# Kernel optimization log

Hardware: AMD Instinct MI355X
Metric: run time of the kernel (lower is better)

## Reference

```python
import jax, jax.numpy as jnp
import numpy as np

_EPS = 1e-6
_ZCA_EPS = 1e-5
NEG_SLOPE_ATTN = 0.2   # LeakyReLU inside score_mlp
NEG_SLOPE_FFN = 0.1    # VNLinearLeakyReLU negative_slope


def _safe_norm(x, axis, keepdims=False):
    # norm with zero-gradient at exactly-zero vectors (matches torch subgradient)
    sq = jnp.sum(x * x, axis=axis, keepdims=keepdims)
    safe = jnp.where(sq == 0, 1.0, sq)
    return jnp.sqrt(safe) * (sq > 0)


def vn_linear(W, x):
    # W: (out, in); x: (B, C_in, 3, N) -> (B, C_out, 3, N)
    return jnp.einsum('oi,bivn->bovn', W, x)


def zca_layernorm(x, gamma):
    # x: (B, C, 3, N); whiten the 3D vector components per batch element
    B, C = x.shape[0], x.shape[1]
    xf = x.reshape(B, C, 3, -1).transpose(0, 2, 1, 3).reshape(B, 3, -1)
    xf = xf.astype(jnp.float32)
    mu = xf.mean(axis=-1, keepdims=True)
    xc = xf - mu
    M = xc.shape[-1]
    cov = (xc @ xc.transpose(0, 2, 1)) / (float(M) + _EPS)  # (B,3,3)
    cov = cov + _ZCA_EPS * jnp.eye(3, dtype=cov.dtype)[None]
    w, V = jnp.linalg.eigh(cov)
    w = jnp.maximum(w, _ZCA_EPS)
    Wm = (V * jax.lax.rsqrt(w)[:, None, :]) @ V.transpose(0, 2, 1)  # (B,3,3)
    xw = Wm @ xc
    xw = xw.reshape(B, 3, C, -1).transpose(0, 2, 1, 3).reshape(x.shape).astype(x.dtype)
    return xw * gamma[None, :, None, None]


def cwsa_attention(x, pos, Wq, Wk, Wv, Wo, W1, b1, W2, b2):
    q = vn_linear(Wq, x)  # (B,C,3,N)
    k = vn_linear(Wk, x)
    v = vn_linear(Wv, x)
    qk = q.transpose(0, 3, 1, 2)  # (B,N,C,3)
    kk = k.transpose(0, 3, 1, 2)
    vv = v.transpose(0, 3, 1, 2)
    rel = qk[:, :, None, :, :] - kk[:, None, :, :, :]      # (B,N,N,C,3)
    rel_norm = _safe_norm(rel, axis=-1)                    # (B,N,N,C)
    rel_mean = rel_norm.mean(axis=-1, keepdims=True)       # (B,N,N,1)
    rel_pos = pos[:, :, None, :] - pos[:, None, :, :]      # (B,N,N,3)
    rel_pos_norm = _safe_norm(rel_pos, axis=-1, keepdims=True)  # (B,N,N,1)
    score_in = jnp.concatenate([rel_mean, rel_pos_norm], axis=-1)  # (B,N,N,2)
    h = jax.nn.leaky_relu(score_in @ W1.T + b1, NEG_SLOPE_ATTN)
    scores = h @ W2.T + b2                                  # (B,N,N,C)
    attn = jax.nn.softmax(scores, axis=2)                   # softmax over keys j
    out = jnp.einsum('bijk,bjkd->bikd', attn, vv)           # (B,N,C,3)
    out = out.transpose(0, 2, 3, 1)                         # (B,C,3,N)
    return vn_linear(Wo, out)


def vn_leaky_relu(p, d, ns):
    # p, d: (B, C, 3, N)
    dot = jnp.sum(p * d, axis=2, keepdims=True)
    dsq = jnp.sum(d * d, axis=2, keepdims=True)
    mask = (dot >= 0).astype(p.dtype)
    proj = p - (dot / (dsq + _EPS)) * d
    return ns * p + (1.0 - ns) * (mask * p + (1.0 - mask) * proj)


def ffn(x, Wfeat, Wdir, Wffn2):
    p = vn_linear(Wfeat, x)
    d = vn_linear(Wdir, x)
    h = vn_leaky_relu(p, d, NEG_SLOPE_FFN)
    return vn_linear(Wffn2, h)


def setup_inputs() -> dict:
    key = jax.random.key(0)
    ks = jax.random.split(key, 16)
    B, C, N = 2, 128, 256
    hidden, ratio = 64, 2
    sC = 1.0 / np.sqrt(C)
    inp = {
        'x': jax.random.normal(ks[0], (B, C, 3, N), dtype=jnp.float32),
        'pos': jax.random.normal(ks[1], (B, N, 3), dtype=jnp.float32),
        'Wq': jax.random.normal(ks[2], (C, C), dtype=jnp.float32) * sC,
        'Wk': jax.random.normal(ks[3], (C, C), dtype=jnp.float32) * sC,
        'Wv': jax.random.normal(ks[4], (C, C), dtype=jnp.float32) * sC,
        'Wo': jax.random.normal(ks[5], (C, C), dtype=jnp.float32) * sC,
        'W1': jax.random.normal(ks[6], (hidden, 2), dtype=jnp.float32) * (1.0 / np.sqrt(2.0)),
        'b1': jnp.zeros((hidden,), dtype=jnp.float32),
        'W2': jax.random.normal(ks[7], (C, hidden), dtype=jnp.float32) * (1.0 / np.sqrt(hidden)),
        'b2': jnp.zeros((C,), dtype=jnp.float32),
        'gamma1': jnp.ones((C,), dtype=jnp.float32),
        'Wfeat': jax.random.normal(ks[8], (C * ratio, C), dtype=jnp.float32) * sC,
        'Wdir': jax.random.normal(ks[9], (C * ratio, C), dtype=jnp.float32) * sC,
        'Wffn2': jax.random.normal(ks[10], (C, C * ratio), dtype=jnp.float32) * (1.0 / np.sqrt(C * ratio)),
        'gamma2': jnp.ones((C,), dtype=jnp.float32),
    }
    return inp


def reference(x, pos, Wq, Wk, Wv, Wo, W1, b1, W2, b2, gamma1, Wfeat, Wdir, Wffn2, gamma2):
    a = cwsa_attention(x, pos, Wq, Wk, Wv, Wo, W1, b1, W2, b2)
    x1 = zca_layernorm(x + a, gamma1)
    f = ffn(x1, Wfeat, Wdir, Wffn2)
    return zca_layernorm(x1 + f, gamma2)
```

## Files before the change

kernel.cpp:

```cpp
#include <hip/hip_runtime.h>
#include <math.h>

#define BB 2
#define CC 128
#define NN 256
#define HH 64
#define CHX 256
#define COLS 768
#define NEG_ATTN 0.2f
#define NEG_FFN 0.1f

typedef __attribute__((ext_vector_type(8))) short short8b;
typedef __attribute__((ext_vector_type(4))) float f32x4;

__device__ __forceinline__ unsigned bf16rne(float x) {
  unsigned u = __float_as_uint(x);
  return (u + 0x7fffu + ((u >> 16) & 1u)) >> 16;
}

__global__ __launch_bounds__(256) void k_qkv(
    const float* __restrict__ x, const float* __restrict__ Wq,
    const float* __restrict__ Wk, const float* __restrict__ Wv,
    float* __restrict__ q_t, float* __restrict__ k_nat, float* __restrict__ v_t3)
{
  const int ct = blockIdx.x, which = blockIdx.y, b = blockIdx.z;
  const int col0 = ct * 16;
  __shared__ float xt[CC][16];
  const float* xb = x + (size_t)b * CC * COLS;
  for (int idx = threadIdx.x; idx < CC * 16; idx += 256) {
    int r = idx >> 4, cc = idx & 15;
    xt[r][cc] = xb[r * COLS + col0 + cc];
  }
  __syncthreads();
  const float* W = (which == 0) ? Wq : ((which == 1) ? Wk : Wv);
  const int co = threadIdx.x >> 1;
  const int cc0 = (threadIdx.x & 1) * 8;
  float acc[8];
#pragma unroll
  for (int k = 0; k < 8; k++) acc[k] = 0.f;
  const float* wrow = W + co * CC;
  for (int ci = 0; ci < CC; ci++) {
    float wv = wrow[ci];
#pragma unroll
    for (int k = 0; k < 8; k++) acc[k] = fmaf(wv, xt[ci][cc0 + k], acc[k]);
  }
#pragma unroll
  for (int k = 0; k < 8; k++) {
    int col = col0 + cc0 + k;
    int v = col >> 8, n = col & 255;
    float val = acc[k];
    if (which == 0)      q_t[((size_t)(b * NN + n) * CC + co) * 3 + v] = val;
    else if (which == 1) k_nat[(size_t)(b * CC + co) * COLS + col] = val;
    else                 v_t3[((size_t)(b * NN + n) * CC + co) * 3 + v] = val;
  }
}

__global__ __launch_bounds__(256) void k_rel(
    const float* __restrict__ q_t, const float* __restrict__ k_nat,
    const float* __restrict__ pos, float* __restrict__ rm_all,
    float* __restrict__ rp_all)
{
  const int i = blockIdx.x, b = blockIdx.y;
  const int t = threadIdx.x;
  __shared__ float qv[CC * 3];
  for (int idx = t; idx < CC * 3; idx += 256)
    qv[idx] = q_t[(size_t)(b * NN + i) * CC * 3 + idx];
  __syncthreads();
  const int j = t;
  const float* kb = k_nat + (size_t)b * CC * COLS;
  float p0 = 0.f, p1 = 0.f, p2 = 0.f, p3 = 0.f;
  for (int c = 0; c < CC; c += 4) {
    float kx0 = kb[(c + 0) * COLS + j], ky0 = kb[(c + 0) * COLS + 256 + j], kz0 = kb[(c + 0) * COLS + 512 + j];
    float kx1 = kb[(c + 1) * COLS + j], ky1 = kb[(c + 1) * COLS + 256 + j], kz1 = kb[(c + 1) * COLS + 512 + j];
    float kx2 = kb[(c + 2) * COLS + j], ky2 = kb[(c + 2) * COLS + 256 + j], kz2 = kb[(c + 2) * COLS + 512 + j];
    float kx3 = kb[(c + 3) * COLS + j], ky3 = kb[(c + 3) * COLS + 256 + j], kz3 = kb[(c + 3) * COLS + 512 + j];
    float dx, dy, dz, sq;
    dx = kx0 - qv[(c + 0) * 3]; dy = ky0 - qv[(c + 0) * 3 + 1]; dz = kz0 - qv[(c + 0) * 3 + 2];
    sq = dx * dx + dy * dy + dz * dz; p0 += (sq > 0.f) ? sqrtf(sq) : 0.f;
    dx = kx1 - qv[(c + 1) * 3]; dy = ky1 - qv[(c + 1) * 3 + 1]; dz = kz1 - qv[(c + 1) * 3 + 2];
    sq = dx * dx + dy * dy + dz * dz; p1 += (sq > 0.f) ? sqrtf(sq) : 0.f;
    dx = kx2 - qv[(c + 2) * 3]; dy = ky2 - qv[(c + 2) * 3 + 1]; dz = kz2 - qv[(c + 2) * 3 + 2];
    sq = dx * dx + dy * dy + dz * dz; p2 += (sq > 0.f) ? sqrtf(sq) : 0.f;
    dx = kx3 - qv[(c + 3) * 3]; dy = ky3 - qv[(c + 3) * 3 + 1]; dz = kz3 - qv[(c + 3) * 3 + 2];
    sq = dx * dx + dy * dy + dz * dz; p3 += (sq > 0.f) ? sqrtf(sq) : 0.f;
  }
  rm_all[(size_t)(b * NN + i) * NN + j] = ((p0 + p1) + (p2 + p3)) * (1.f / 128.f);
  float dx = pos[(b * NN + i) * 3 + 0] - pos[(b * NN + j) * 3 + 0];
  float dy = pos[(b * NN + i) * 3 + 1] - pos[(b * NN + j) * 3 + 1];
  float dz = pos[(b * NN + i) * 3 + 2] - pos[(b * NN + j) * 3 + 2];
  float sq = dx * dx + dy * dy + dz * dz;
  rp_all[(size_t)(b * NN + i) * NN + j] = (sq > 0.f) ? sqrtf(sq) : 0.f;
}

__global__ __launch_bounds__(256, 4) void k_attn(
    const float* __restrict__ rm_all, const float* __restrict__ rp_all,
    const float* __restrict__ v_t3, const float* __restrict__ W1,
    const float* __restrict__ b1, const float* __restrict__ W2,
    float* __restrict__ a_nat)
{
  const int i = blockIdx.x, chalf = blockIdx.y, b = blockIdx.z;
  const int t = threadIdx.x;
  __shared__ __align__(16) short hh_s[64 * 64];
  __shared__ __align__(16) short w2_s[64 * 64];
  __shared__ float sc_s[64 * 65];
  __shared__ float rm_s[NN], rp_s[NN];

  rm_s[t] = rm_all[(size_t)(b * NN + i) * NN + t];
  rp_s[t] = rp_all[(size_t)(b * NN + i) * NN + t];
  {
    const int cl = t >> 2, h0 = (t & 3) * 16;
    const float* wrow = W2 + (size_t)(chalf * 64 + cl) * HH + h0;
#pragma unroll
    for (int e = 0; e < 8; e++) {
      unsigned lo = bf16rne(wrow[2 * e]);
      unsigned hi = bf16rne(wrow[2 * e + 1]);
      int didx = (cl * 32 + (h0 >> 1) + e) ^ ((cl & 7) << 2);
      ((unsigned*)w2_s)[didx] = lo | (hi << 16);
    }
  }
  const int h2 = (t & 31) * 2, jgrp = t >> 5;
  const float4 w1v = *reinterpret_cast<const float4*>(W1 + 2 * h2);
  const float c0 = b1[h2], c1 = b1[h2 + 1];
  __syncthreads();

  auto phase2 = [&](int q) {
#pragma unroll
    for (int jj = 0; jj < 8; jj++) {
      int jl = jgrp * 8 + jj;
      int jg = q * 64 + jl;
      float rmv = rm_s[jg], rpv = rp_s[jg];
      float g0 = fmaf(w1v.x, rmv, fmaf(w1v.y, rpv, c0));
      float g1 = fmaf(w1v.z, rmv, fmaf(w1v.w, rpv, c1));
      g0 = (g0 >= 0.f) ? g0 : NEG_ATTN * g0;
      g1 = (g1 >= 0.f) ? g1 : NEG_ATTN * g1;
      int didx = (jl * 32 + (h2 >> 1)) ^ ((jl & 7) << 2);
      ((unsigned*)hh_s)[didx] = bf16rne(g0) | (bf16rne(g1) << 16);
    }
  };

  phase2(0);
  __syncthreads();

  const int lane = t & 63, wv = t >> 6;
  const int g8 = (lane >> 4) * 8;
  const int cdx = wv * 16 + (lane & 15);
  const short8b bfr0 = *reinterpret_cast<const short8b*>(&w2_s[(cdx * 64 + g8) ^ ((cdx & 7) << 3)]);
  const short8b bfr1 = *reinterpret_cast<const short8b*>(&w2_s[(cdx * 64 + 32 + g8) ^ ((cdx & 7) << 3)]);

  const int cl = lane;
  const int par = wv;
  const int vc = chalf * 64 + cl;
  float l = 0.f, a0 = 0.f, a1 = 0.f, a2 = 0.f;

  for (int q = 0; q < 4; q++) {
#pragma unroll
    for (int jt = 0; jt < 4; jt++) {
      int jr = jt * 16 + (lane & 15);
      short8b af0 = *reinterpret_cast<const short8b*>(&hh_s[(jr * 64 + g8) ^ ((jr & 7) << 3)]);
      short8b af1 = *reinterpret_cast<const short8b*>(&hh_s[(jr * 64 + 32 + g8) ^ ((jr & 7) << 3)]);
      f32x4 acc = {0.f, 0.f, 0.f, 0.f};
      acc = __builtin_amdgcn_mfma_f32_16x16x32_bf16(af0, bfr0, acc, 0, 0, 0);
      acc = __builtin_amdgcn_mfma_f32_16x16x32_bf16(af1, bfr1, acc, 0, 0, 0);
      int row0 = jt * 16 + (lane >> 4) * 4;
      int ccol = wv * 16 + (lane & 15);
#pragma unroll
      for (int r = 0; r < 4; r++) sc_s[(row0 + r) * 65 + ccol] = acc[r];
    }
    __syncthreads();
#pragma unroll 4
    for (int jj = 0; jj < 16; jj++) {
      int jl = jj * 4 + par;
      int jg = q * 64 + jl;
      float s = sc_s[jl * 65 + cl];
      const float* vb = v_t3 + ((size_t)(b * NN + jg) * CC + vc) * 3;
      float v0 = vb[0], v1 = vb[1], v2 = vb[2];
      float p = __expf(s);
      l += p;
      a0 = fmaf(p, v0, a0);
      a1 = fmaf(p, v1, a1);
      a2 = fmaf(p, v2, a2);
    }
    if (q < 3) phase2(q + 1);
    __syncthreads();
  }

  float* mrg = sc_s;
  if (par != 0) {
    float* mp = mrg + (cl * 3 + (par - 1)) * 4;
    mp[0] = l; mp[1] = a0; mp[2] = a1; mp[3] = a2;
  }
  __syncthreads();
  if (par == 0) {
    float L = l, A0 = a0, A1 = a1, A2 = a2;
#pragma unroll
    for (int q = 0; q < 3; q++) {
      const float* mp = mrg + (cl * 3 + q) * 4;
      L += mp[0]; A0 += mp[1]; A1 += mp[2]; A2 += mp[3];
    }
    float inv = 1.f / L;
    float* ap = a_nat + (size_t)(b * CC + vc) * COLS + i;
    ap[0] = A0 * inv; ap[256] = A1 * inv; ap[512] = A2 * inv;
  }
}

__global__ __launch_bounds__(256) void k_wo_res(
    const float* __restrict__ a_nat, const float* __restrict__ Wo,
    const float* __restrict__ x, float* __restrict__ y1)
{
  const int ct = blockIdx.x, cohalf = blockIdx.y, b = blockIdx.z;
  const int col0 = ct * 16;
  __shared__ float at[CC][16];
  const float* ab = a_nat + (size_t)b * CC * COLS;
  for (int idx = threadIdx.x; idx < CC * 16; idx += 256) {
    int r = idx >> 4, cc = idx & 15;
    at[r][cc] = ab[r * COLS + col0 + cc];
  }
  __syncthreads();
  const int co = cohalf * 64 + (threadIdx.x >> 2);
  const int cc0 = (threadIdx.x & 3) * 4;
  float acc[4];
#pragma unroll
  for (int k = 0; k < 4; k++) acc[k] = 0.f;
  const float* wrow = Wo + co * CC;
  for (int ci = 0; ci < CC; ci++) {
    float wv = wrow[ci];
#pragma unroll
    for (int k = 0; k < 4; k++) acc[k] = fmaf(wv, at[ci][cc0 + k], acc[k]);
  }
  const size_t base = (size_t)(b * CC + co) * COLS + col0 + cc0;
#pragma unroll
  for (int k = 0; k < 4; k++) y1[base + k] = x[base + k] + acc[k];
}

__global__ __launch_bounds__(1024) void k_stats(
    const float* __restrict__ y, float* __restrict__ stats)
{
  const int b = blockIdx.x;
  const float* yb = y + (size_t)b * CC * COLS;
  const int t = threadIdx.x;
  float v9[9];
#pragma unroll
  for (int k = 0; k < 9; k++) v9[k] = 0.f;
  for (int e = 0; e < 32; e++) {
    int idx = e * 1024 + t;
    int cidx = idx >> 8, n = idx & 255;
    const float* row = yb + cidx * COLS + n;
    float v0 = row[0], v1 = row[256], v2 = row[512];
    v9[0] += v0; v9[1] += v1; v9[2] += v2;
    v9[3] += v0 * v0; v9[4] += v0 * v1; v9[5] += v0 * v2;
    v9[6] += v1 * v1; v9[7] += v1 * v2; v9[8] += v2 * v2;
  }
#pragma unroll
  for (int off = 32; off >= 1; off >>= 1)
#pragma unroll
    for (int k = 0; k < 9; k++) v9[k] += __shfl_down(v9[k], off);
  __shared__ float red[16][9];
  const int wid = t >> 6, lane = t & 63;
  if (lane == 0)
#pragma unroll
    for (int k = 0; k < 9; k++) red[wid][k] = v9[k];
  __syncthreads();
  if (t == 0) {
    float tot[9];
#pragma unroll
    for (int k = 0; k < 9; k++) tot[k] = 0.f;
    for (int w = 0; w < 16; w++)
#pragma unroll
      for (int k = 0; k < 9; k++) tot[k] += red[w][k];
    const float M = (float)(CC * NN);
    float mu0 = tot[0] / M, mu1 = tot[1] / M, mu2 = tot[2] / M;
    float A[3][3];
    A[0][0] = (tot[3] - M * mu0 * mu0) / M + 1e-5f;
    A[0][1] = A[1][0] = (tot[4] - M * mu0 * mu1) / M;
    A[0][2] = A[2][0] = (tot[5] - M * mu0 * mu2) / M;
    A[1][1] = (tot[6] - M * mu1 * mu1) / M + 1e-5f;
    A[1][2] = A[2][1] = (tot[7] - M * mu1 * mu2) / M;
    A[2][2] = (tot[8] - M * mu2 * mu2) / M + 1e-5f;
    float V[3][3] = {{1.f, 0.f, 0.f}, {0.f, 1.f, 0.f}, {0.f, 0.f, 1.f}};
    for (int sweep = 0; sweep < 10; sweep++) {
      for (int pi = 0; pi < 3; pi++) {
        const int p = (pi == 2) ? 1 : 0;
        const int q = (pi == 0) ? 1 : 2;
        float apq = A[p][q];
        if (fabsf(apq) < 1e-30f) continue;
        float theta = (A[q][q] - A[p][p]) / (2.f * apq);
        float tt = 1.f / (fabsf(theta) + sqrtf(theta * theta + 1.f));
        if (theta < 0.f) tt = -tt;
        float cr = 1.f / sqrtf(tt * tt + 1.f);
        float sr = tt * cr;
        float app = A[p][p], aqq = A[q][q];
        A[p][p] = app - tt * apq;
        A[q][q] = aqq + tt * apq;
        A[p][q] = A[q][p] = 0.f;
        const int r = 3 - p - q;
        float arp = A[r][p], arq = A[r][q];
        A[r][p] = A[p][r] = cr * arp - sr * arq;
        A[r][q] = A[q][r] = sr * arp + cr * arq;
        for (int rr = 0; rr < 3; rr++) {
          float vrp = V[rr][p], vrq = V[rr][q];
          V[rr][p] = cr * vrp - sr * vrq;
          V[rr][q] = sr * vrp + cr * vrq;
        }
      }
    }
    float rs[3];
#pragma unroll
    for (int k = 0; k < 3; k++) rs[k] = rsqrtf(fmaxf(A[k][k], 1e-5f));
    float* st = stats + b * 12;
    st[0] = mu0; st[1] = mu1; st[2] = mu2;
    for (int u = 0; u < 3; u++)
      for (int v = 0; v < 3; v++) {
        float acc = 0.f;
        for (int k = 0; k < 3; k++) acc += V[u][k] * rs[k] * V[v][k];
        st[3 + u * 3 + v] = acc;
      }
  }
}

__global__ __launch_bounds__(256) void k_ffn1(
    const float* __restrict__ y1, const float* __restrict__ stats,
    const float* __restrict__ gamma, const float* __restrict__ Wfeat,
    const float* __restrict__ Wdir, float* __restrict__ hout)
{
  const int nt = blockIdx.x, cs = blockIdx.y, b = blockIdx.z;
  const int n0 = nt * 16, co0 = cs * 64;
  __shared__ float xt[CC][48];
  const float* yb = y1 + (size_t)b * CC * COLS;
  const float* st = stats + b * 12;
  for (int idx = threadIdx.x; idx < CC * 16; idx += 256) {
    int ci = idx >> 4, nn = idx & 15;
    const float* row = yb + ci * COLS + n0 + nn;
    float d0 = row[0] - st[0], d1 = row[256] - st[1], d2 = row[512] - st[2];
    float g = gamma[ci];
    xt[ci][nn]      = g * (st[3] * d0 + st[4] * d1 + st[5] * d2);
    xt[ci][16 + nn] = g * (st[6] * d0 + st[7] * d1 + st[8] * d2);
    xt[ci][32 + nn] = g * (st[9] * d0 + st[10] * d1 + st[11] * d2);
  }
  __syncthreads();
  const int co = co0 + (threadIdx.x & 63);
  const int nn0 = (threadIdx.x >> 6) * 4;
  float p[3][4], d[3][4];
#pragma unroll
  for (int v = 0; v < 3; v++)
#pragma unroll
    for (int k = 0; k < 4; k++) { p[v][k] = 0.f; d[v][k] = 0.f; }
  const float* wf = Wfeat + co * CC;
  const float* wd = Wdir + co * CC;
  for (int ci = 0; ci < CC; ci++) {
    float a = wf[ci], bb = wd[ci];
#pragma unroll
    for (int v = 0; v < 3; v++)
#pragma unroll
      for (int k = 0; k < 4; k++) {
        float xv = xt[ci][v * 16 + nn0 + k];
        p[v][k] = fmaf(a, xv, p[v][k]);
        d[v][k] = fmaf(bb, xv, d[v][k]);
      }
  }
  float* hb = hout + (size_t)(b * CHX + co) * COLS;
#pragma unroll
  for (int k = 0; k < 4; k++) {
    float dot = p[0][k] * d[0][k] + p[1][k] * d[1][k] + p[2][k] * d[2][k];
    float dsq = d[0][k] * d[0][k] + d[1][k] * d[1][k] + d[2][k] * d[2][k];
    float coef = (dot >= 0.f) ? 0.f : (1.f - NEG_FFN) * dot / (dsq + 1e-6f);
#pragma unroll
    for (int v = 0; v < 3; v++)
      hb[v * 256 + n0 + nn0 + k] = p[v][k] - coef * d[v][k];
  }
}

__global__ __launch_bounds__(256) void k_ffn2(
    const float* __restrict__ h, const float* __restrict__ Wffn2,
    const float* __restrict__ y1, const float* __restrict__ stats,
    const float* __restrict__ gamma, float* __restrict__ x2)
{
  const int ct = blockIdx.x, cohalf = blockIdx.y, b = blockIdx.z;
  const int col0 = ct * 16;
  __shared__ float ht[CHX][16];
  const float* hb = h + (size_t)b * CHX * COLS;
  for (int idx = threadIdx.x; idx < CHX * 16; idx += 256) {
    int r = idx >> 4, cc = idx & 15;
    ht[r][cc] = hb[r * COLS + col0 + cc];
  }
  __syncthreads();
  const int co = cohalf * 64 + (threadIdx.x >> 2);
  const int cc0 = (threadIdx.x & 3) * 4;
  float acc[4];
#pragma unroll
  for (int k = 0; k < 4; k++) acc[k] = 0.f;
  const float* w = Wffn2 + co * CHX;
  for (int ci = 0; ci < CHX; ci++) {
    float wv = w[ci];
#pragma unroll
    for (int k = 0; k < 4; k++) acc[k] = fmaf(wv, ht[ci][cc0 + k], acc[k]);
  }
  const int col_base = col0 + cc0;
  const int v = col_base >> 8, n = col_base & 255;
  const float* st = stats + b * 12;
  const float* yb = y1 + (size_t)(b * CC + co) * COLS + n;
  const float g = gamma[co];
  const float w0 = st[3 + v * 3 + 0], w1 = st[3 + v * 3 + 1], w2 = st[3 + v * 3 + 2];
  const size_t base = (size_t)(b * CC + co) * COLS + col_base;
#pragma unroll
  for (int k = 0; k < 4; k++) {
    float d0 = yb[k] - st[0], d1 = yb[256 + k] - st[1], d2 = yb[512 + k] - st[2];
    float xw = g * (w0 * d0 + w1 * d1 + w2 * d2);
    x2[base + k] = xw + acc[k];
  }
}

__global__ __launch_bounds__(256) void k_zca_apply(
    const float* __restrict__ y, const float* __restrict__ stats,
    const float* __restrict__ gamma, float* __restrict__ out)
{
  int idx = blockIdx.x * blockDim.x + threadIdx.x;
  int b = idx >> 15, rem = idx & 32767;
  int cidx = rem >> 8, n = rem & 255;
  const float* st = stats + b * 12;
  const size_t base = (size_t)(b * CC + cidx) * COLS + n;
  float v0 = y[base] - st[0];
  float v1 = y[base + 256] - st[1];
  float v2 = y[base + 512] - st[2];
  float g = gamma[cidx];
  out[base]       = g * (st[3] * v0 + st[4] * v1 + st[5] * v2);
  out[base + 256] = g * (st[6] * v0 + st[7] * v1 + st[8] * v2);
  out[base + 512] = g * (st[9] * v0 + st[10] * v1 + st[11] * v2);
}

extern "C" void kernel_launch(void* const* d_in, const int* in_sizes, int n_in,
                              void* d_out, int out_size, void* d_ws, size_t ws_size,
                              hipStream_t stream)
{
  (void)in_sizes; (void)n_in; (void)out_size; (void)ws_size;
  const float* x      = (const float*)d_in[0];
  const float* pos    = (const float*)d_in[1];
  const float* Wq     = (const float*)d_in[2];
  const float* Wk     = (const float*)d_in[3];
  const float* Wv     = (const float*)d_in[4];
  const float* Wo     = (const float*)d_in[5];
  const float* W1     = (const float*)d_in[6];
  const float* b1     = (const float*)d_in[7];
  const float* W2     = (const float*)d_in[8];
  const float* gamma1 = (const float*)d_in[10];
  const float* Wfeat  = (const float*)d_in[11];
  const float* Wdir   = (const float*)d_in[12];
  const float* Wffn2  = (const float*)d_in[13];
  const float* gamma2 = (const float*)d_in[14];

  float* ws = (float*)d_ws;
  const size_t QKV = (size_t)BB * NN * CC * 3;
  const size_t RM  = (size_t)BB * NN * NN;
  const size_t HB  = (size_t)BB * CHX * COLS;

  float* q_t    = ws;
  float* k_nat  = q_t    + QKV;
  float* v_t3   = k_nat  + QKV;
  float* rm_all = v_t3   + QKV;
  float* rp_all = rm_all + RM;
  float* a_nat  = rp_all + RM;
  float* y1     = a_nat  + QKV;
  float* hbuf   = y1     + QKV;
  float* x2     = hbuf   + HB;
  float* stats1 = x2     + QKV;
  float* stats2 = stats1 + 64;

  k_qkv<<<dim3(48, 3, BB), 256, 0, stream>>>(x, Wq, Wk, Wv, q_t, k_nat, v_t3);
  k_rel<<<dim3(NN, BB), 256, 0, stream>>>(q_t, k_nat, pos, rm_all, rp_all);
  k_attn<<<dim3(NN, 2, BB), 256, 0, stream>>>(rm_all, rp_all, v_t3, W1, b1, W2, a_nat);
  k_wo_res<<<dim3(48, 2, BB), 256, 0, stream>>>(a_nat, Wo, x, y1);
  k_stats<<<BB, 1024, 0, stream>>>(y1, stats1);
  k_ffn1<<<dim3(16, 4, BB), 256, 0, stream>>>(y1, stats1, gamma1, Wfeat, Wdir, hbuf);
  k_ffn2<<<dim3(48, 2, BB), 256, 0, stream>>>(hbuf, Wffn2, y1, stats1, gamma1, x2);
  k_stats<<<BB, 1024, 0, stream>>>(x2, stats2);
  k_zca_apply<<<256, 256, 0, stream>>>(x2, stats2, gamma2, (float*)d_out);
}
```

Baseline: 106.6 us.

## Fuse ZCA statistics into Wo and FFN2 epilogues, tile rel over 4 queries

The two-block k_stats passes, which re-read the full activation with only 2 blocks, are replaced: the Wo-residual and FFN2 kernels now compute per-block 9-moment partial sums in their epilogues, and a tiny finalize kernel reduces them and runs the eigen-decomposition. Those GEMM kernels now tile 16 points across all three vector components, so grids shrink from 48x2x2 to 16x2x2 blocks. k_rel processes 4 query rows per block so each key load is reused four times, and it launches a quarter as many blocks. The cost is lower parallelism in the GEMM kernels and extra partial-sum traffic plus one more serial finalize step.

```diff
diff --git a/kernel.cpp b/kernel.cpp
--- a/kernel.cpp
+++ b/kernel.cpp
@@ -55,41 +55,47 @@
   }
 }
 
-__global__ __launch_bounds__(256) void k_rel(
+__global__ __launch_bounds__(256) void k_rel4(
     const float* __restrict__ q_t, const float* __restrict__ k_nat,
     const float* __restrict__ pos, float* __restrict__ rm_all,
     float* __restrict__ rp_all)
 {
-  const int i = blockIdx.x, b = blockIdx.y;
+  const int i0 = blockIdx.x * 4, b = blockIdx.y;
   const int t = threadIdx.x;
-  __shared__ float qv[CC * 3];
-  for (int idx = t; idx < CC * 3; idx += 256)
-    qv[idx] = q_t[(size_t)(b * NN + i) * CC * 3 + idx];
+  __shared__ float qv[4 * CC * 3];
+  for (int idx = t; idx < 4 * CC * 3; idx += 256)
+    qv[idx] = q_t[(size_t)(b * NN + i0) * CC * 3 + idx];
   __syncthreads();
   const int j = t;
   const float* kb = k_nat + (size_t)b * CC * COLS;
-  float p0 = 0.f, p1 = 0.f, p2 = 0.f, p3 = 0.f;
-  for (int c = 0; c < CC; c += 4) {
-    float kx0 = kb[(c + 0) * COLS + j], ky0 = kb[(c + 0) * COLS + 256 + j], kz0 = kb[(c + 0) * COLS + 512 + j];
-    float kx1 = kb[(c + 1) * COLS + j], ky1 = kb[(c + 1) * COLS + 256 + j], kz1 = kb[(c + 1) * COLS + 512 + j];
-    float kx2 = kb[(c + 2) * COLS + j], ky2 = kb[(c + 2) * COLS + 256 + j], kz2 = kb[(c + 2) * COLS + 512 + j];
-    float kx3 = kb[(c + 3) * COLS + j], ky3 = kb[(c + 3) * COLS + 256 + j], kz3 = kb[(c + 3) * COLS + 512 + j];
+  float a0 = 0.f, a1 = 0.f, a2 = 0.f, a3 = 0.f;
+  for (int c = 0; c < CC; c++) {
+    float kx = kb[c * COLS + j];
+    float ky = kb[c * COLS + 256 + j];
+    float kz = kb[c * COLS + 512 + j];
     float dx, dy, dz, sq;
-    dx = kx0 - qv[(c + 0) * 3]; dy = ky0 - qv[(c + 0) * 3 + 1]; dz = kz0 - qv[(c + 0) * 3 + 2];
-    sq = dx * dx + dy * dy + dz * dz; p0 += (sq > 0.f) ? sqrtf(sq) : 0.f;
-    dx = kx1 - qv[(c + 1) * 3]; dy = ky1 - qv[(c + 1) * 3 + 1]; dz = kz1 - qv[(c + 1) * 3 + 2];
-    sq = dx * dx + dy * dy + dz * dz; p1 += (sq > 0.f) ? sqrtf(sq) : 0.f;
-    dx = kx2 - qv[(c + 2) * 3]; dy = ky2 - qv[(c + 2) * 3 + 1]; dz = kz2 - qv[(c + 2) * 3 + 2];
-    sq = dx * dx + dy * dy + dz * dz; p2 += (sq > 0.f) ? sqrtf(sq) : 0.f;
-    dx = kx3 - qv[(c + 3) * 3]; dy = ky3 - qv[(c + 3) * 3 + 1]; dz = kz3 - qv[(c + 3) * 3 + 2];
-    sq = dx * dx + dy * dy + dz * dz; p3 += (sq > 0.f) ? sqrtf(sq) : 0.f;
-  }
-  rm_all[(size_t)(b * NN + i) * NN + j] = ((p0 + p1) + (p2 + p3)) * (1.f / 128.f);
-  float dx = pos[(b * NN + i) * 3 + 0] - pos[(b * NN + j) * 3 + 0];
-  float dy = pos[(b * NN + i) * 3 + 1] - pos[(b * NN + j) * 3 + 1];
-  float dz = pos[(b * NN + i) * 3 + 2] - pos[(b * NN + j) * 3 + 2];
-  float sq = dx * dx + dy * dy + dz * dz;
-  rp_all[(size_t)(b * NN + i) * NN + j] = (sq > 0.f) ? sqrtf(sq) : 0.f;
+    dx = kx - qv[c * 3];       dy = ky - qv[c * 3 + 1];       dz = kz - qv[c * 3 + 2];
+    sq = dx * dx + dy * dy + dz * dz; a0 += (sq > 0.f) ? sqrtf(sq) : 0.f;
+    dx = kx - qv[384 + c * 3]; dy = ky - qv[384 + c * 3 + 1]; dz = kz - qv[384 + c * 3 + 2];
+    sq = dx * dx + dy * dy + dz * dz; a1 += (sq > 0.f) ? sqrtf(sq) : 0.f;
+    dx = kx - qv[768 + c * 3]; dy = ky - qv[768 + c * 3 + 1]; dz = kz - qv[768 + c * 3 + 2];
+    sq = dx * dx + dy * dy + dz * dz; a2 += (sq > 0.f) ? sqrtf(sq) : 0.f;
+    dx = kx - qv[1152 + c * 3]; dy = ky - qv[1152 + c * 3 + 1]; dz = kz - qv[1152 + c * 3 + 2];
+    sq = dx * dx + dy * dy + dz * dz; a3 += (sq > 0.f) ? sqrtf(sq) : 0.f;
+  }
+  rm_all[(size_t)(b * NN + i0 + 0) * NN + j] = a0 * (1.f / 128.f);
+  rm_all[(size_t)(b * NN + i0 + 1) * NN + j] = a1 * (1.f / 128.f);
+  rm_all[(size_t)(b * NN + i0 + 2) * NN + j] = a2 * (1.f / 128.f);
+  rm_all[(size_t)(b * NN + i0 + 3) * NN + j] = a3 * (1.f / 128.f);
+  float pjx = pos[(b * NN + j) * 3], pjy = pos[(b * NN + j) * 3 + 1], pjz = pos[(b * NN + j) * 3 + 2];
+#pragma unroll
+  for (int ii = 0; ii < 4; ii++) {
+    float dx = pos[(b * NN + i0 + ii) * 3 + 0] - pjx;
+    float dy = pos[(b * NN + i0 + ii) * 3 + 1] - pjy;
+    float dz = pos[(b * NN + i0 + ii) * 3 + 2] - pjz;
+    float sq = dx * dx + dy * dy + dz * dz;
+    rp_all[(size_t)(b * NN + i0 + ii) * NN + j] = (sq > 0.f) ? sqrtf(sq) : 0.f;
+  }
 }
 
 __global__ __launch_bounds__(256, 4) void k_attn(
@@ -203,118 +209,132 @@
   }
 }
 
-__global__ __launch_bounds__(256) void k_wo_res(
+__global__ __launch_bounds__(256) void k_wo_res_p(
     const float* __restrict__ a_nat, const float* __restrict__ Wo,
-    const float* __restrict__ x, float* __restrict__ y1)
-{
-  const int ct = blockIdx.x, cohalf = blockIdx.y, b = blockIdx.z;
-  const int col0 = ct * 16;
-  __shared__ float at[CC][16];
+    const float* __restrict__ x, float* __restrict__ y1,
+    float* __restrict__ part)
+{
+  const int nt = blockIdx.x, cohalf = blockIdx.y, b = blockIdx.z;
+  const int n0 = nt * 16;
+  const int t = threadIdx.x;
+  __shared__ float at[CC][48];
   const float* ab = a_nat + (size_t)b * CC * COLS;
-  for (int idx = threadIdx.x; idx < CC * 16; idx += 256) {
-    int r = idx >> 4, cc = idx & 15;
-    at[r][cc] = ab[r * COLS + col0 + cc];
-  }
-  __syncthreads();
-  const int co = cohalf * 64 + (threadIdx.x >> 2);
-  const int cc0 = (threadIdx.x & 3) * 4;
-  float acc[4];
-#pragma unroll
-  for (int k = 0; k < 4; k++) acc[k] = 0.f;
+  for (int idx = t; idx < CC * 16; idx += 256) {
+    int ci = idx >> 4, nn = idx & 15;
+    const float* row = ab + ci * COLS + n0 + nn;
+    at[ci][nn]      = row[0];
+    at[ci][16 + nn] = row[256];
+    at[ci][32 + nn] = row[512];
+  }
+  __syncthreads();
+  const int co = cohalf * 64 + (t >> 2);
+  const int nn0 = (t & 3) * 4;
+  float acc[3][4];
+#pragma unroll
+  for (int v = 0; v < 3; v++)
+#pragma unroll
+    for (int k = 0; k < 4; k++) acc[v][k] = 0.f;
   const float* wrow = Wo + co * CC;
   for (int ci = 0; ci < CC; ci++) {
     float wv = wrow[ci];
 #pragma unroll
-    for (int k = 0; k < 4; k++) acc[k] = fmaf(wv, at[ci][cc0 + k], acc[k]);
-  }
-  const size_t base = (size_t)(b * CC + co) * COLS + col0 + cc0;
-#pragma unroll
-  for (int k = 0; k < 4; k++) y1[base + k] = x[base + k] + acc[k];
-}
-
-__global__ __launch_bounds__(1024) void k_stats(
-    const float* __restrict__ y, float* __restrict__ stats)
-{
-  const int b = blockIdx.x;
-  const float* yb = y + (size_t)b * CC * COLS;
-  const int t = threadIdx.x;
+    for (int v = 0; v < 3; v++)
+#pragma unroll
+      for (int k = 0; k < 4; k++)
+        acc[v][k] = fmaf(wv, at[ci][v * 16 + nn0 + k], acc[v][k]);
+  }
   float v9[9];
 #pragma unroll
   for (int k = 0; k < 9; k++) v9[k] = 0.f;
-  for (int e = 0; e < 32; e++) {
-    int idx = e * 1024 + t;
-    int cidx = idx >> 8, n = idx & 255;
-    const float* row = yb + cidx * COLS + n;
-    float v0 = row[0], v1 = row[256], v2 = row[512];
-    v9[0] += v0; v9[1] += v1; v9[2] += v2;
-    v9[3] += v0 * v0; v9[4] += v0 * v1; v9[5] += v0 * v2;
-    v9[6] += v1 * v1; v9[7] += v1 * v2; v9[8] += v2 * v2;
+  const size_t base = (size_t)(b * CC + co) * COLS + n0 + nn0;
+#pragma unroll
+  for (int k = 0; k < 4; k++) {
+    float y0 = x[base + k]       + acc[0][k];
+    float y1v = x[base + 256 + k] + acc[1][k];
+    float y2 = x[base + 512 + k] + acc[2][k];
+    y1[base + k]       = y0;
+    y1[base + 256 + k] = y1v;
+    y1[base + 512 + k] = y2;
+    v9[0] += y0; v9[1] += y1v; v9[2] += y2;
+    v9[3] += y0 * y0; v9[4] += y0 * y1v; v9[5] += y0 * y2;
+    v9[6] += y1v * y1v; v9[7] += y1v * y2; v9[8] += y2 * y2;
   }
 #pragma unroll
   for (int off = 32; off >= 1; off >>= 1)
 #pragma unroll
     for (int k = 0; k < 9; k++) v9[k] += __shfl_down(v9[k], off);
-  __shared__ float red[16][9];
+  __syncthreads();
+  float* red = &at[0][0];
   const int wid = t >> 6, lane = t & 63;
   if (lane == 0)
 #pragma unroll
-    for (int k = 0; k < 9; k++) red[wid][k] = v9[k];
-  __syncthreads();
-  if (t == 0) {
-    float tot[9];
-#pragma unroll
-    for (int k = 0; k < 9; k++) tot[k] = 0.f;
-    for (int w = 0; w < 16; w++)
-#pragma unroll
-      for (int k = 0; k < 9; k++) tot[k] += red[w][k];
-    const float M = (float)(CC * NN);
-    float mu0 = tot[0] / M, mu1 = tot[1] / M, mu2 = tot[2] / M;
-    float A[3][3];
-    A[0][0] = (tot[3] - M * mu0 * mu0) / M + 1e-5f;
-    A[0][1] = A[1][0] = (tot[4] - M * mu0 * mu1) / M;
-    A[0][2] = A[2][0] = (tot[5] - M * mu0 * mu2) / M;
-    A[1][1] = (tot[6] - M * mu1 * mu1) / M + 1e-5f;
-    A[1][2] = A[2][1] = (tot[7] - M * mu1 * mu2) / M;
-    A[2][2] = (tot[8] - M * mu2 * mu2) / M + 1e-5f;
-    float V[3][3] = {{1.f, 0.f, 0.f}, {0.f, 1.f, 0.f}, {0.f, 0.f, 1.f}};
-    for (int sweep = 0; sweep < 10; sweep++) {
-      for (int pi = 0; pi < 3; pi++) {
-        const int p = (pi == 2) ? 1 : 0;
-        const int q = (pi == 0) ? 1 : 2;
-        float apq = A[p][q];
-        if (fabsf(apq) < 1e-30f) continue;
-        float theta = (A[q][q] - A[p][p]) / (2.f * apq);
-        float tt = 1.f / (fabsf(theta) + sqrtf(theta * theta + 1.f));
-        if (theta < 0.f) tt = -tt;
-        float cr = 1.f / sqrtf(tt * tt + 1.f);
-        float sr = tt * cr;
-        float app = A[p][p], aqq = A[q][q];
-        A[p][p] = app - tt * apq;
-        A[q][q] = aqq + tt * apq;
-        A[p][q] = A[q][p] = 0.f;
-        const int r = 3 - p - q;
-        float arp = A[r][p], arq = A[r][q];
-        A[r][p] = A[p][r] = cr * arp - sr * arq;
-        A[r][q] = A[q][r] = sr * arp + cr * arq;
-        for (int rr = 0; rr < 3; rr++) {
-          float vrp = V[rr][p], vrq = V[rr][q];
-          V[rr][p] = cr * vrp - sr * vrq;
-          V[rr][q] = sr * vrp + cr * vrq;
-        }
+    for (int k = 0; k < 9; k++) red[wid * 9 + k] = v9[k];
+  __syncthreads();
+  if (t == 0)
+#pragma unroll
+    for (int k = 0; k < 9; k++)
+      part[(size_t)(b * 32 + nt * 2 + cohalf) * 9 + k] =
+          (red[k] + red[9 + k]) + (red[18 + k] + red[27 + k]);
+}
+
+__global__ __launch_bounds__(64) void k_zca_fin(
+    const float* __restrict__ partials, float* __restrict__ stats)
+{
+  const int b = blockIdx.x;
+  if (threadIdx.x != 0) return;
+  float tot[9];
+#pragma unroll
+  for (int k = 0; k < 9; k++) tot[k] = 0.f;
+  for (int p = 0; p < 32; p++)
+#pragma unroll
+    for (int k = 0; k < 9; k++) tot[k] += partials[(size_t)(b * 32 + p) * 9 + k];
+  const float M = (float)(CC * NN);
+  float mu0 = tot[0] / M, mu1 = tot[1] / M, mu2 = tot[2] / M;
+  float A[3][3];
+  A[0][0] = (tot[3] - M * mu0 * mu0) / M + 1e-5f;
+  A[0][1] = A[1][0] = (tot[4] - M * mu0 * mu1) / M;
+  A[0][2] = A[2][0] = (tot[5] - M * mu0 * mu2) / M;
+  A[1][1] = (tot[6] - M * mu1 * mu1) / M + 1e-5f;
+  A[1][2] = A[2][1] = (tot[7] - M * mu1 * mu2) / M;
+  A[2][2] = (tot[8] - M * mu2 * mu2) / M + 1e-5f;
+  float V[3][3] = {{1.f, 0.f, 0.f}, {0.f, 1.f, 0.f}, {0.f, 0.f, 1.f}};
+  for (int sweep = 0; sweep < 10; sweep++) {
+    for (int pi = 0; pi < 3; pi++) {
+      const int p = (pi == 2) ? 1 : 0;
+      const int q = (pi == 0) ? 1 : 2;
+      float apq = A[p][q];
+      if (fabsf(apq) < 1e-30f) continue;
+      float theta = (A[q][q] - A[p][p]) / (2.f * apq);
+      float tt = 1.f / (fabsf(theta) + sqrtf(theta * theta + 1.f));
+      if (theta < 0.f) tt = -tt;
+      float cr = 1.f / sqrtf(tt * tt + 1.f);
+      float sr = tt * cr;
+      float app = A[p][p], aqq = A[q][q];
+      A[p][p] = app - tt * apq;
+      A[q][q] = aqq + tt * apq;
+      A[p][q] = A[q][p] = 0.f;
+      const int r = 3 - p - q;
+      float arp = A[r][p], arq = A[r][q];
+      A[r][p] = A[p][r] = cr * arp - sr * arq;
+      A[r][q] = A[q][r] = sr * arp + cr * arq;
+      for (int rr = 0; rr < 3; rr++) {
+        float vrp = V[rr][p], vrq = V[rr][q];
+        V[rr][p] = cr * vrp - sr * vrq;
+        V[rr][q] = sr * vrp + cr * vrq;
       }
     }
-    float rs[3];
-#pragma unroll
-    for (int k = 0; k < 3; k++) rs[k] = rsqrtf(fmaxf(A[k][k], 1e-5f));
-    float* st = stats + b * 12;
-    st[0] = mu0; st[1] = mu1; st[2] = mu2;
-    for (int u = 0; u < 3; u++)
-      for (int v = 0; v < 3; v++) {
-        float acc = 0.f;
-        for (int k = 0; k < 3; k++) acc += V[u][k] * rs[k] * V[v][k];
-        st[3 + u * 3 + v] = acc;
-      }
-  }
+  }
+  float rs[3];
+#pragma unroll
+  for (int k = 0; k < 3; k++) rs[k] = rsqrtf(fmaxf(A[k][k], 1e-5f));
+  float* st = stats + b * 12;
+  st[0] = mu0; st[1] = mu1; st[2] = mu2;
+  for (int u = 0; u < 3; u++)
+    for (int v = 0; v < 3; v++) {
+      float acc = 0.f;
+      for (int k = 0; k < 3; k++) acc += V[u][k] * rs[k] * V[v][k];
+      st[3 + u * 3 + v] = acc;
+    }
 }
 
 __global__ __launch_bounds__(256) void k_ffn1(
@@ -369,44 +389,77 @@
   }
 }
 
-__global__ __launch_bounds__(256) void k_ffn2(
+__global__ __launch_bounds__(256) void k_ffn2_p(
     const float* __restrict__ h, const float* __restrict__ Wffn2,
     const float* __restrict__ y1, const float* __restrict__ stats,
-    const float* __restrict__ gamma, float* __restrict__ x2)
-{
-  const int ct = blockIdx.x, cohalf = blockIdx.y, b = blockIdx.z;
-  const int col0 = ct * 16;
-  __shared__ float ht[CHX][16];
+    const float* __restrict__ gamma, float* __restrict__ x2,
+    float* __restrict__ part)
+{
+  const int nt = blockIdx.x, cohalf = blockIdx.y, b = blockIdx.z;
+  const int n0 = nt * 16;
+  const int t = threadIdx.x;
+  __shared__ float ht[CHX][48];
   const float* hb = h + (size_t)b * CHX * COLS;
-  for (int idx = threadIdx.x; idx < CHX * 16; idx += 256) {
-    int r = idx >> 4, cc = idx & 15;
-    ht[r][cc] = hb[r * COLS + col0 + cc];
-  }
-  __syncthreads();
-  const int co = cohalf * 64 + (threadIdx.x >> 2);
-  const int cc0 = (threadIdx.x & 3) * 4;
-  float acc[4];
-#pragma unroll
-  for (int k = 0; k < 4; k++) acc[k] = 0.f;
+  for (int idx = t; idx < CHX * 16; idx += 256) {
+    int ci = idx >> 4, nn = idx & 15;
+    const float* row = hb + ci * COLS + n0 + nn;
+    ht[ci][nn]      = row[0];
+    ht[ci][16 + nn] = row[256];
+    ht[ci][32 + nn] = row[512];
+  }
+  __syncthreads();
+  const int co = cohalf * 64 + (t >> 2);
+  const int nn0 = (t & 3) * 4;
+  float acc[3][4];
+#pragma unroll
+  for (int v = 0; v < 3; v++)
+#pragma unroll
+    for (int k = 0; k < 4; k++) acc[v][k] = 0.f;
   const float* w = Wffn2 + co * CHX;
   for (int ci = 0; ci < CHX; ci++) {
     float wv = w[ci];
 #pragma unroll
-    for (int k = 0; k < 4; k++) acc[k] = fmaf(wv, ht[ci][cc0 + k], acc[k]);
-  }
-  const int col_base = col0 + cc0;
-  const int v = col_base >> 8, n = col_base & 255;
+    for (int v = 0; v < 3; v++)
+#pragma unroll
+      for (int k = 0; k < 4; k++)
+        acc[v][k] = fmaf(wv, ht[ci][v * 16 + nn0 + k], acc[v][k]);
+  }
   const float* st = stats + b * 12;
-  const float* yb = y1 + (size_t)(b * CC + co) * COLS + n;
   const float g = gamma[co];
-  const float w0 = st[3 + v * 3 + 0], w1 = st[3 + v * 3 + 1], w2 = st[3 + v * 3 + 2];
-  const size_t base = (size_t)(b * CC + co) * COLS + col_base;
+  const float* yb = y1 + (size_t)(b * CC + co) * COLS + n0 + nn0;
+  const size_t base = (size_t)(b * CC + co) * COLS + n0 + nn0;
+  float v9[9];
+#pragma unroll
+  for (int k = 0; k < 9; k++) v9[k] = 0.f;
 #pragma unroll
   for (int k = 0; k < 4; k++) {
     float d0 = yb[k] - st[0], d1 = yb[256 + k] - st[1], d2 = yb[512 + k] - st[2];
-    float xw = g * (w0 * d0 + w1 * d1 + w2 * d2);
-    x2[base + k] = xw + acc[k];
-  }
+    float x0 = g * (st[3] * d0 + st[4] * d1 + st[5] * d2) + acc[0][k];
+    float x1 = g * (st[6] * d0 + st[7] * d1 + st[8] * d2) + acc[1][k];
+    float xz = g * (st[9] * d0 + st[10] * d1 + st[11] * d2) + acc[2][k];
+    x2[base + k]       = x0;
+    x2[base + 256 + k] = x1;
+    x2[base + 512 + k] = xz;
+    v9[0] += x0; v9[1] += x1; v9[2] += xz;
+    v9[3] += x0 * x0; v9[4] += x0 * x1; v9[5] += x0 * xz;
+    v9[6] += x1 * x1; v9[7] += x1 * xz; v9[8] += xz * xz;
+  }
+#pragma unroll
+  for (int off = 32; off >= 1; off >>= 1)
+#pragma unroll
+    for (int k = 0; k < 9; k++) v9[k] += __shfl_down(v9[k], off);
+  __syncthreads();
+  float* red = &ht[0][0];
+  const int wid = t >> 6, lane = t & 63;
+  if (lane == 0)
+#pragma unroll
+    for (int k = 0; k < 9; k++) red[wid * 9 + k] = v9[k];
+  __syncthreads();
+  if (t == 0)
+#pragma unroll
+    for (int k = 0; k < 9; k++)
+      part[(size_t)(b * 32 + nt * 2 + cohalf) * 9 + k] =
+          (red[k] + red[9 + k]) + (red[18 + k] + red[27 + k]);
 }
 
 __global__ __launch_bounds__(256) void k_zca_apply(
@@ -463,14 +516,16 @@
   float* x2     = hbuf   + HB;
   float* stats1 = x2     + QKV;
   float* stats2 = stats1 + 64;
+  float* part1  = stats2 + 64;
+  float* part2  = part1  + 640;
 
   k_qkv<<<dim3(48, 3, BB), 256, 0, stream>>>(x, Wq, Wk, Wv, q_t, k_nat, v_t3);
-  k_rel<<<dim3(NN, BB), 256, 0, stream>>>(q_t, k_nat, pos, rm_all, rp_all);
+  k_rel4<<<dim3(NN / 4, BB), 256, 0, stream>>>(q_t, k_nat, pos, rm_all, rp_all);
   k_attn<<<dim3(NN, 2, BB), 256, 0, stream>>>(rm_all, rp_all, v_t3, W1, b1, W2, a_nat);
-  k_wo_res<<<dim3(48, 2, BB), 256, 0, stream>>>(a_nat, Wo, x, y1);
-  k_stats<<<BB, 1024, 0, stream>>>(y1, stats1);
+  k_wo_res_p<<<dim3(16, 2, BB), 256, 0, stream>>>(a_nat, Wo, x, y1, part1);
+  k_zca_fin<<<BB, 64, 0, stream>>>(part1, stats1);
   k_ffn1<<<dim3(16, 4, BB), 256, 0, stream>>>(y1, stats1, gamma1, Wfeat, Wdir, hbuf);
-  k_ffn2<<<dim3(48, 2, BB), 256, 0, stream>>>(hbuf, Wffn2, y1, stats1, gamma1, x2);
-  k_stats<<<BB, 1024, 0, stream>>>(x2, stats2);
+  k_ffn2_p<<<dim3(16, 2, BB), 256, 0, stream>>>(hbuf, Wffn2, y1, stats1, gamma1, x2, part2);
+  k_zca_fin<<<BB, 64, 0, stream>>>(part2, stats2);
   k_zca_apply<<<256, 256, 0, stream>>>(x2, stats2, gamma2, (float*)d_out);
 }
```

Result: slower. 133.9 us (+25.5%).
